# Performance work log

Hardware: AMD Instinct MI355X
Metric: run time of the kernel (lower is better)

The kernel has to match this reference:

```python
import jax, jax.numpy as jnp
import numpy as np

THRESHOLD_P = 0.4  # nucleus_select default threshold_p


def setup_inputs() -> dict:
    key = jax.random.key(0)
    B, N = 512, 50257
    logits = jax.random.normal(key, (B, N), dtype=jnp.float32)
    # nucleus_select consumes softmax weights (rows sum to 1)
    weights = jax.nn.softmax(logits, axis=-1)
    return {"weights": weights}


def reference(weights):
    """Batched nucleus (top-p) selection, jit-compatible padded form.

    Returns:
      sorted_idx: (B, N) int32  -- indices of weights sorted descending
      norm_w:     (B, N) f32    -- renormalized selected weights in sorted
                                   order; positions >= k are exactly 0
      k:          (B,)   int32  -- nucleus size per sample (>= 1)
    For sample b the torch module's outputs are sorted_idx[b, :k[b]] and
    norm_w[b, :k[b]].
    """
    B, N = weights.shape
    # descending sort (values + original indices)
    sorted_idx = jnp.argsort(-weights, axis=-1)
    sorted_w = jnp.take_along_axis(weights, sorted_idx, axis=-1)
    cumsum = jnp.cumsum(sorted_w, axis=-1)
    exceeded = cumsum > THRESHOLD_P
    # first position where cumsum > p, then +1; if never exceeded, keep all N
    first = jnp.argmax(exceeded, axis=-1).astype(jnp.int32)
    k = jnp.where(jnp.any(exceeded, axis=-1), first + 1, jnp.int32(N))
    k = jnp.maximum(k, 1)
    keep = jnp.arange(N, dtype=jnp.int32)[None, :] < k[:, None]  # (B, N)
    sel_w = sorted_w * keep.astype(sorted_w.dtype)
    norm_w = sel_w / jnp.sum(sel_w, axis=-1, keepdims=True)
    return sorted_idx.astype(jnp.int32), norm_w, k
```

## Files before the change

### kernel.cpp

```cpp
#include <hip/hip_runtime.h>
#include <stdint.h>

#define B    512
#define N    50257
#define BLK  512
#define NWAVE 8
#define TILE 5632
#define CHUNK 704
#define NGRP 11
#define THRESH 0.4f

__device__ __forceinline__ uint32_t sort_key(float w) { return ~__float_as_uint(w); }

__device__ __forceinline__ void hist_elem(uint32_t* hw0, const float w) {
    const uint32_t key = sort_key(w);
    atomicAdd(hw0 + (key & 255u), 1u);
    atomicAdd(hw0 + 256 + ((key >> 8) & 255u), 1u);
    atomicAdd(hw0 + 512 + ((key >> 16) & 255u), 1u);
    atomicAdd(hw0 + 768 + ((key >> 24) & 255u), 1u);
}

__global__ __launch_bounds__(BLK) void hist4_fast(const float* __restrict__ wts,
                                                  uint32_t* __restrict__ histWS) {
    __shared__ uint32_t hw[NWAVE][4][256];
    __shared__ uint32_t wtot[4];
    const int row = blockIdx.x;
    const size_t base = (size_t)row * N;
    const int tid = threadIdx.x;
    const int lane = tid & 63;
    const int wv = tid >> 6;

    {
        uint32_t* p = &hw[wv][0][0];
        for (int j = lane; j < 4 * 256; j += 64) p[j] = 0;
    }
    uint32_t* hw0 = &hw[wv][0][0];

    const int head = (int)((4 - (base & 3)) & 3);
    for (int i = tid; i < head; i += BLK) hist_elem(hw0, wts[base + i]);
    const int nvec = (N - head) >> 2;
    const float4* v4 = (const float4*)(wts + base + head);
    for (int iv = tid; iv < nvec; iv += BLK) {
        const float4 f = v4[iv];
        hist_elem(hw0, f.x); hist_elem(hw0, f.y);
        hist_elem(hw0, f.z); hist_elem(hw0, f.w);
    }
    for (int i = head + 4 * nvec + tid; i < N; i += BLK) hist_elem(hw0, wts[base + i]);
    __syncthreads();

    for (int p = 0; p < 4; ++p) {
        uint32_t cnt = 0;
        if (tid < 256) {
            #pragma unroll
            for (int w = 0; w < NWAVE; ++w) cnt += hw[w][p][tid];
        }
        uint32_t incl = cnt;
        #pragma unroll
        for (int o = 1; o < 64; o <<= 1) {
            const uint32_t u = __shfl_up(incl, o);
            if (lane >= o) incl += u;
        }
        if (tid < 256 && lane == 63) wtot[tid >> 6] = incl;
        __syncthreads();
        if (tid < 256) {
            uint32_t prefix = 0;
            const int w4 = tid >> 6;
            #pragma unroll
            for (int w2 = 0; w2 < 4; ++w2) if (w2 < w4) prefix += wtot[w2];
            histWS[((size_t)row * 4 + p) * 256 + tid] = prefix + incl - cnt;
        }
        __syncthreads();
    }
}

template <int SHIFT, bool FIRST, bool LAST>
__global__ __launch_bounds__(BLK, 4) void scatter_pl(const float* __restrict__ wts,
                                                     const unsigned long long* __restrict__ src,
                                                     unsigned long long* __restrict__ dst,
                                                     uint32_t* __restrict__ outIdx,
                                                     float* __restrict__ outW,
                                                     const uint32_t* __restrict__ histWS) {
    __shared__ __align__(16) unsigned long long stage[TILE];
    __shared__ uint16_t waveCnt[NWAVE][256];
    __shared__ uint32_t delta[256];
    __shared__ uint32_t wtot[4];

    const int row = blockIdx.x;
    const size_t base = (size_t)row * N;
    const int tid  = threadIdx.x;
    const int lane = tid & 63;
    const int wv   = tid >> 6;
    constexpr int PASS = SHIFT / 8;
    constexpr int KS = SHIFT + 16;

    uint32_t curReg = 0;
    if (tid < 256) curReg = histWS[((size_t)row * 4 + PASS) * 256 + tid];

    const int numTiles = (N + TILE - 1) / TILE;

    unsigned long long pairN[NGRP];
    {
        const int cb = wv * CHUNK;
        #pragma unroll
        for (int g = 0; g < NGRP; ++g) {
            const int i = cb + g * 64 + lane;
            pairN[g] = FIRST ? (((unsigned long long)sort_key(wts[base + i]) << 16) | (uint32_t)i)
                             : src[base + i];
        }
    }

    for (int t = 0; t < numTiles; ++t) {
        const int tbase = t * TILE;
        const int tileLen = (N - tbase < TILE) ? (N - tbase) : TILE;
        const int cbase = tbase + wv * CHUNK;
        const bool full = (tbase + TILE <= N);

        {
            uint2* z = (uint2*)&waveCnt[wv][0];
            z[lane] = make_uint2(0u, 0u);
        }
        unsigned long long pairR[NGRP];
        uint32_t posR[NGRP];
        #pragma unroll
        for (int g = 0; g < NGRP; ++g) pairR[g] = pairN[g];

        if (full) {
            #pragma unroll
            for (int g = 0; g < NGRP; ++g) {
                const uint32_t d = (uint32_t)(pairR[g] >> KS) & 255u;
                unsigned long long peers = ~0ull;
                #pragma unroll
                for (int bb = 0; bb < 8; ++bb) {
                    const unsigned long long bit = __ballot((d >> bb) & 1u);
                    peers &= ((d >> bb) & 1u) ? bit : ~bit;
                }
                const unsigned long long lower = peers & ((1ull << lane) - 1ull);
                const uint32_t cnt = (uint32_t)waveCnt[wv][d];
                posR[g] = cnt + (uint32_t)__popcll(lower);
                if (lower == 0ull) waveCnt[wv][d] = (uint16_t)(cnt + (uint32_t)__popcll(peers));
            }
        } else {
            #pragma unroll
            for (int g = 0; g < NGRP; ++g) {
                const int i = cbase + g * 64 + lane;
                const bool valid = (i < N);
                const uint32_t d = (uint32_t)(pairR[g] >> KS) & 255u;
                unsigned long long peers = __ballot(valid);
                #pragma unroll
                for (int bb = 0; bb < 8; ++bb) {
                    const unsigned long long bit = __ballot((d >> bb) & 1u);
                    peers &= ((d >> bb) & 1u) ? bit : ~bit;
                }
                const unsigned long long lower = peers & ((1ull << lane) - 1ull);
                uint32_t cnt = 0;
                if (valid) cnt = (uint32_t)waveCnt[wv][d];
                posR[g] = cnt + (uint32_t)__popcll(lower);
                if (valid && lower == 0ull) waveCnt[wv][d] = (uint16_t)(cnt + (uint32_t)__popcll(peers));
            }
        }
        __syncthreads();

        uint32_t run = 0;
        if (tid < 256) {
            #pragma unroll
            for (int w = 0; w < NWAVE; ++w) {
                const uint32_t c = (uint32_t)waveCnt[w][tid];
                waveCnt[w][tid] = (uint16_t)run;
                run += c;
            }
        }
        uint32_t incl = run;
        #pragma unroll
        for (int o = 1; o < 64; o <<= 1) {
            const uint32_t u = __shfl_up(incl, o);
            if (lane >= o) incl += u;
        }
        if (tid < 256 && lane == 63) wtot[tid >> 6] = incl;
        __syncthreads();
        if (tid < 256) {
            uint32_t prefix = 0;
            const int w4 = tid >> 6;
            #pragma unroll
            for (int w2 = 0; w2 < 4; ++w2) if (w2 < w4) prefix += wtot[w2];
            const uint32_t ts = prefix + incl - run;
            delta[tid] = curReg - ts;
            curReg += run;
            #pragma unroll
            for (int w = 0; w < NWAVE; ++w)
                waveCnt[w][tid] = (uint16_t)((uint32_t)waveCnt[w][tid] + ts);
        }
        __syncthreads();

        if (t + 1 < numTiles) {
            const int ncb = (t + 1) * TILE + wv * CHUNK;
            if (ncb + CHUNK <= N) {
                #pragma unroll
                for (int g = 0; g < NGRP; ++g) {
                    const int i = ncb + g * 64 + lane;
                    pairN[g] = FIRST ? (((unsigned long long)sort_key(wts[base + i]) << 16) | (uint32_t)i)
                                     : src[base + i];
                }
            } else {
                #pragma unroll
                for (int g = 0; g < NGRP; ++g) {
                    const int i = ncb + g * 64 + lane;
                    unsigned long long pair = 0;
                    if (i < N)
                        pair = FIRST ? (((unsigned long long)sort_key(wts[base + i]) << 16) | (uint32_t)i)
                                     : src[base + i];
                    pairN[g] = pair;
                }
            }
        }

        if (full) {
            #pragma unroll
            for (int g = 0; g < NGRP; ++g) {
                const uint32_t d = (uint32_t)(pairR[g] >> KS) & 255u;
                stage[(uint32_t)waveCnt[wv][d] + posR[g]] = pairR[g];
            }
        } else {
            #pragma unroll
            for (int g = 0; g < NGRP; ++g) {
                const int i = cbase + g * 64 + lane;
                if (i < N) {
                    const uint32_t d = (uint32_t)(pairR[g] >> KS) & 255u;
                    stage[(uint32_t)waveCnt[wv][d] + posR[g]] = pairR[g];
                }
            }
        }
        __syncthreads();

        const int tileLenEven = tileLen & ~1;
        for (int p0 = 2 * tid; p0 < tileLenEven; p0 += 2 * BLK) {
            const ulonglong2 two = *(const ulonglong2*)&stage[p0];
            const uint32_t d0 = (uint32_t)(two.x >> KS) & 255u;
            const uint32_t d1 = (uint32_t)(two.y >> KS) & 255u;
            const uint32_t g0 = delta[d0] + (uint32_t)p0;
            const uint32_t g1 = delta[d1] + (uint32_t)p0 + 1u;
            if (LAST) {
                outIdx[base + g0] = (uint32_t)(two.x & 0xFFFFull);
                outW[base + g0]   = __uint_as_float(~(uint32_t)(two.x >> 16));
                outIdx[base + g1] = (uint32_t)(two.y & 0xFFFFull);
                outW[base + g1]   = __uint_as_float(~(uint32_t)(two.y >> 16));
            } else {
                dst[base + g0] = two.x;
                dst[base + g1] = two.y;
            }
        }
        for (int p = tileLenEven + tid; p < tileLen; p += BLK) {
            const unsigned long long pair = stage[p];
            const uint32_t d = (uint32_t)(pair >> KS) & 255u;
            const uint32_t g = delta[d] + (uint32_t)p;
            if (LAST) {
                outIdx[base + g] = (uint32_t)(pair & 0xFFFFull);
                outW[base + g]   = __uint_as_float(~(uint32_t)(pair >> 16));
            } else {
                dst[base + g] = pair;
            }
        }
    }
}

__global__ __launch_bounds__(BLK) void finalize_row(float* __restrict__ out0,
                                                    float* __restrict__ out1,
                                                    float* __restrict__ out2) {
    __shared__ float waveSum[NWAVE];
    __shared__ int   waveFirst[NWAVE];
    __shared__ float waveCum[NWAVE];
    __shared__ int   s_k;
    __shared__ float s_total;

    const int row = blockIdx.x;
    const size_t base = (size_t)row * N;
    const int tid  = threadIdx.x;
    const int lane = tid & 63;
    const int wv   = tid >> 6;

    if (tid == 0) { s_k = -1; s_total = 0.f; }
    __syncthreads();

    float carry = 0.f;
    const int numTiles = (N + BLK - 1) / BLK;
    for (int t = 0; t < numTiles; ++t) {
        const int i = t * BLK + tid;
        const bool valid = (i < N);
        float w = valid ? out1[base + i] : 0.f;

        float s = w;
        #pragma unroll
        for (int o = 1; o < 64; o <<= 1) {
            float u = __shfl_up(s, o);
            if (lane >= o) s += u;
        }
        if (lane == 63) waveSum[wv] = s;
        __syncthreads();

        float prefix = 0.f, blockTot = 0.f;
        #pragma unroll
        for (int w2 = 0; w2 < NWAVE; ++w2) {
            float t2 = waveSum[w2];
            if (w2 < wv) prefix += t2;
            blockTot += t2;
        }
        const float cum = carry + prefix + s;

        const bool exceed = valid && (cum > THRESH);
        const unsigned long long bal = __ballot(exceed);
        const int fl = (bal == 0ull) ? 64 : (__ffsll(bal) - 1);
        if (lane == 0) waveFirst[wv] = fl;
        if (fl < 64 && lane == fl) waveCum[wv] = cum;
        __syncthreads();
        if (tid == 0) {
            for (int w2 = 0; w2 < NWAVE; ++w2) {
                if (waveFirst[w2] < 64) {
                    s_k = t * BLK + w2 * 64 + waveFirst[w2] + 1;
                    s_total = waveCum[w2];
                    break;
                }
            }
        }
        __syncthreads();
        if (s_k >= 0) break;
        carry += blockTot;
        __syncthreads();
    }

    int k = s_k;
    float total = s_total;
    if (k < 0) { k = N; total = carry; }
    const float inv = 1.0f / total;

    const uint32_t* idxU = (const uint32_t*)out0;
    const int head = (int)((4 - (base & 3)) & 3);
    const int nvec = (N - head) >> 2;
    const int vend = head + 4 * nvec;

    for (int i = tid; i < head; i += BLK) {
        const uint32_t idx = idxU[base + i];
        const float w = out1[base + i];
        out0[base + i] = (float)idx;
        out1[base + i] = (i < k) ? (w * inv) : 0.f;
    }
    const uint4*  ivp = (const uint4*)(idxU + base + head);
    float4*       o0v = (float4*)(out0 + base + head);
    float4*       o1v = (float4*)(out1 + base + head);
    for (int v = tid; v < nvec; v += BLK) {
        const uint4  iv = ivp[v];
        const float4 wv4 = o1v[v];
        const int i = head + 4 * v;
        float4 o0, o1;
        o0.x = (float)iv.x; o0.y = (float)iv.y; o0.z = (float)iv.z; o0.w = (float)iv.w;
        o1.x = (i + 0 < k) ? wv4.x * inv : 0.f;
        o1.y = (i + 1 < k) ? wv4.y * inv : 0.f;
        o1.z = (i + 2 < k) ? wv4.z * inv : 0.f;
        o1.w = (i + 3 < k) ? wv4.w * inv : 0.f;
        o0v[v] = o0;
        o1v[v] = o1;
    }
    for (int i = vend + tid; i < N; i += BLK) {
        const uint32_t idx = idxU[base + i];
        const float w = out1[base + i];
        out0[base + i] = (float)idx;
        out1[base + i] = (i < k) ? (w * inv) : 0.f;
    }
    if (tid == 0) out2[row] = (float)k;
}

#define NSUB (TILE / BLK)

template <int SHIFT, bool FIRST, bool LAST>
__global__ __launch_bounds__(BLK, 4) void scatter_tile(const float* __restrict__ wts,
                                                       const uint32_t* __restrict__ keySrc,
                                                       const uint16_t* __restrict__ idxSrc,
                                                       uint32_t* __restrict__ keyDst,
                                                       uint16_t* __restrict__ idxDst,
                                                       uint32_t* __restrict__ outIdx,
                                                       float* __restrict__ outW,
                                                       const uint32_t* __restrict__ histWS) {
    __shared__ uint32_t stageKey[TILE];
    __shared__ uint16_t stageIdx[TILE];
    __shared__ uint32_t waveCnt32[NWAVE][256];
    __shared__ uint16_t subOff[NSUB][256];
    __shared__ uint32_t cursor[256];
    __shared__ uint32_t tileCnt[256];
    __shared__ uint32_t tileStart[256];
    __shared__ uint32_t scanb[256];

    const int row = blockIdx.x;
    const size_t base = (size_t)row * N;
    const int tid  = threadIdx.x;
    const int lane = tid & 63;
    const int wv   = tid >> 6;
    constexpr int PASS = SHIFT / 8;

    if (tid < 256) cursor[tid] = histWS[((size_t)row * 4 + PASS) * 256 + tid];

    const int numTiles = (N + TILE - 1) / TILE;
    for (int t = 0; t < numTiles; ++t) {
        const int tbase = t * TILE;
        const int tileLen = (N - tbase < TILE) ? (N - tbase) : TILE;

        uint32_t keyR[NSUB];
        uint32_t idxR[NSUB];
        uint32_t posR[NSUB];

        #pragma unroll
        for (int s = 0; s < NSUB; ++s) {
            for (int j = tid; j < NWAVE * 256; j += BLK) ((uint32_t*)waveCnt32)[j] = 0;
            __syncthreads();

            const int i = tbase + s * BLK + tid;
            const bool valid = (i < N);
            uint32_t key = 0, idx = 0, d = 0;
            if (valid) {
                if (FIRST) { key = sort_key(wts[base + i]); idx = (uint32_t)i; }
                else       { key = keySrc[base + i]; idx = (uint32_t)idxSrc[base + i]; }
                d = (key >> SHIFT) & 255u;
            }
            keyR[s] = key;
            if (!FIRST) idxR[s] = idx;

            unsigned long long peers = __ballot(valid);
            #pragma unroll
            for (int b = 0; b < 8; ++b) {
                unsigned long long bit = __ballot(valid && ((d >> b) & 1u));
                peers &= ((d >> b) & 1u) ? bit : ~bit;
            }
            const unsigned long long lower = peers & ((1ull << lane) - 1ull);
            const uint32_t rank = (uint32_t)__popcll(lower);
            if (valid && lower == 0ull) waveCnt32[wv][d] = (uint32_t)__popcll(peers);
            __syncthreads();

            if (tid < 256) {
                uint32_t x = 0;
                #pragma unroll
                for (int w = 0; w < NWAVE; ++w) {
                    uint32_t c = waveCnt32[w][tid];
                    waveCnt32[w][tid] = x;
                    x += c;
                }
                subOff[s][tid] = (uint16_t)x;
            }
            __syncthreads();

            posR[s] = valid ? (waveCnt32[wv][d] + rank) : 0u;
            __syncthreads();
        }

        if (tid < 256) {
            uint32_t run = 0;
            #pragma unroll
            for (int s = 0; s < NSUB; ++s) {
                uint32_t c = subOff[s][tid];
                subOff[s][tid] = (uint16_t)run;
                run += c;
            }
            tileCnt[tid] = run;
            scanb[tid] = run;
        }
        __syncthreads();
        for (int off = 1; off < 256; off <<= 1) {
            uint32_t add = 0;
            if (tid < 256 && tid >= off) add = scanb[tid - off];
            __syncthreads();
            if (tid < 256) scanb[tid] += add;
            __syncthreads();
        }
        if (tid < 256) tileStart[tid] = (tid == 0) ? 0u : scanb[tid - 1];
        __syncthreads();

        #pragma unroll
        for (int s = 0; s < NSUB; ++s) {
            const int i = tbase + s * BLK + tid;
            if (i < N) {
                const uint32_t d = (keyR[s] >> SHIFT) & 255u;
                const uint32_t pos = tileStart[d] + (uint32_t)subOff[s][d] + posR[s];
                stageKey[pos] = keyR[s];
                stageIdx[pos] = (uint16_t)(FIRST ? (uint32_t)i : idxR[s]);
            }
        }
        __syncthreads();

        for (int p = tid; p < tileLen; p += BLK) {
            const uint32_t k = stageKey[p];
            const uint32_t d = (k >> SHIFT) & 255u;
            const uint32_t g = cursor[d] + (uint32_t)p - tileStart[d];
            if (LAST) {
                outIdx[base + g] = (uint32_t)stageIdx[p];
                outW[base + g]   = __uint_as_float(~k);
            } else {
                keyDst[base + g] = k;
                idxDst[base + g] = stageIdx[p];
            }
        }
        __syncthreads();
        if (tid < 256) cursor[tid] += tileCnt[tid];
        __syncthreads();
    }
}

template <int SHIFT>
__global__ __launch_bounds__(BLK) void radix_pass_fb(const float* __restrict__ wts,
                                                     const uint32_t* __restrict__ src,
                                                     uint32_t* __restrict__ dst) {
    __shared__ uint32_t hist[256];
    __shared__ uint32_t scanb[256];
    __shared__ uint32_t running[256];
    __shared__ uint32_t waveCnt32[NWAVE][256];

    const int row = blockIdx.x;
    const size_t base = (size_t)row * N;
    const int tid  = threadIdx.x;
    const int lane = tid & 63;
    const int wv   = tid >> 6;

    if (tid < 256) hist[tid] = 0;
    __syncthreads();
    for (int i = tid; i < N; i += BLK) {
        uint32_t idx = (SHIFT == 0) ? (uint32_t)i : src[base + i];
        uint32_t d = (sort_key(wts[base + idx]) >> SHIFT) & 255u;
        atomicAdd(&hist[d], 1u);
    }
    __syncthreads();

    if (tid < 256) scanb[tid] = hist[tid];
    __syncthreads();
    for (int off = 1; off < 256; off <<= 1) {
        uint32_t add = 0;
        if (tid < 256 && tid >= off) add = scanb[tid - off];
        __syncthreads();
        if (tid < 256) scanb[tid] += add;
        __syncthreads();
    }
    if (tid < 256) running[tid] = (tid == 0) ? 0u : scanb[tid - 1];
    __syncthreads();

    const int numTiles = (N + BLK - 1) / BLK;
    for (int t = 0; t < numTiles; ++t) {
        for (int j = tid; j < NWAVE * 256; j += BLK) ((uint32_t*)waveCnt32)[j] = 0;
        __syncthreads();

        const int i = t * BLK + tid;
        const bool valid = (i < N);
        uint32_t idx = 0, d = 0;
        if (valid) {
            idx = (SHIFT == 0) ? (uint32_t)i : src[base + i];
            d = (sort_key(wts[base + idx]) >> SHIFT) & 255u;
        }
        unsigned long long peers = __ballot(valid);
        #pragma unroll
        for (int b = 0; b < 8; ++b) {
            unsigned long long bit = __ballot(valid && ((d >> b) & 1u));
            peers &= ((d >> b) & 1u) ? bit : ~bit;
        }
        const unsigned long long lower = peers & ((1ull << lane) - 1ull);
        const uint32_t rank = (uint32_t)__popcll(lower);
        if (valid && lower == 0ull) waveCnt32[wv][d] = (uint32_t)__popcll(peers);
        __syncthreads();

        if (tid < 256) {
            uint32_t s = running[tid];
            #pragma unroll
            for (int w = 0; w < NWAVE; ++w) {
                uint32_t c = waveCnt32[w][tid];
                waveCnt32[w][tid] = s;
                s += c;
            }
            running[tid] = s;
        }
        __syncthreads();

        if (valid) {
            uint32_t pos = waveCnt32[wv][d] + rank;
            dst[base + pos] = idx;
        }
        __syncthreads();
    }
}

__global__ __launch_bounds__(BLK) void finalize_fb(const float* __restrict__ wts,
                                                   const uint32_t* __restrict__ sidx,
                                                   float* __restrict__ out0,
                                                   float* __restrict__ out1,
                                                   float* __restrict__ out2) {
    __shared__ float waveSum[NWAVE];
    __shared__ int   waveFirst[NWAVE];
    __shared__ float waveCum[NWAVE];
    __shared__ int   s_k;
    __shared__ float s_total;

    const int row = blockIdx.x;
    const size_t base = (size_t)row * N;
    const int tid  = threadIdx.x;
    const int lane = tid & 63;
    const int wv   = tid >> 6;

    if (tid == 0) { s_k = -1; s_total = 0.f; }
    __syncthreads();

    float carry = 0.f;
    const int numTiles = (N + BLK - 1) / BLK;
    for (int t = 0; t < numTiles; ++t) {
        const int i = t * BLK + tid;
        const bool valid = (i < N);
        float w = valid ? wts[base + sidx[base + i]] : 0.f;

        float s = w;
        #pragma unroll
        for (int o = 1; o < 64; o <<= 1) {
            float u = __shfl_up(s, o);
            if (lane >= o) s += u;
        }
        if (lane == 63) waveSum[wv] = s;
        __syncthreads();

        float prefix = 0.f, blockTot = 0.f;
        #pragma unroll
        for (int w2 = 0; w2 < NWAVE; ++w2) {
            float t2 = waveSum[w2];
            if (w2 < wv) prefix += t2;
            blockTot += t2;
        }
        const float cum = carry + prefix + s;

        const bool exceed = valid && (cum > THRESH);
        const unsigned long long bal = __ballot(exceed);
        const int fl = (bal == 0ull) ? 64 : (__ffsll(bal) - 1);
        if (lane == 0) waveFirst[wv] = fl;
        if (fl < 64 && lane == fl) waveCum[wv] = cum;
        __syncthreads();
        if (tid == 0) {
            for (int w2 = 0; w2 < NWAVE; ++w2) {
                if (waveFirst[w2] < 64) {
                    s_k = t * BLK + w2 * 64 + waveFirst[w2] + 1;
                    s_total = waveCum[w2];
                    break;
                }
            }
        }
        __syncthreads();
        if (s_k >= 0) break;
        carry += blockTot;
        __syncthreads();
    }

    int k = s_k;
    float total = s_total;
    if (k < 0) { k = N; total = carry; }

    for (int i = tid; i < N; i += BLK) {
        const uint32_t idx = sidx[base + i];
        const float w = wts[base + idx];
        out0[base + i] = (float)idx;
        out1[base + i] = (i < k) ? (w / total) : 0.f;
    }
    if (tid == 0) out2[row] = (float)k;
}


extern "C" void kernel_launch(void* const* d_in, const int* in_sizes, int n_in,
                              void* d_out, int out_size, void* d_ws, size_t ws_size,
                              hipStream_t stream) {
    const float* wts = (const float*)d_in[0];
    float* out0 = (float*)d_out;
    float* out1 = out0 + (size_t)B * N;
    float* out2 = out0 + 2 * (size_t)B * N;

    const size_t PAIR_BYTES = (size_t)B * N * 8;
    const size_t KEY_BYTES  = (size_t)B * N * 4;
    const size_t IDX_BYTES  = (size_t)B * N * 2;
    const size_t HIST_BYTES = (size_t)B * 4 * 256 * 4;
    const size_t WS_A = PAIR_BYTES + HIST_BYTES;
    const size_t WS_B = KEY_BYTES + IDX_BYTES + HIST_BYTES;

    dim3 g(B), b(BLK);
    if (ws_size >= WS_A) {
        uint8_t* ws = (uint8_t*)d_ws;
        unsigned long long* pairWS  = (unsigned long long*)ws;
        uint32_t*           histWS  = (uint32_t*)(ws + PAIR_BYTES);
        unsigned long long* pairOUT = (unsigned long long*)d_out;

        hist4_fast<<<g, b, 0, stream>>>(wts, histWS);
        scatter_pl<0,  true,  false><<<g, b, 0, stream>>>(wts, nullptr, pairWS, nullptr, nullptr, histWS);
        scatter_pl<8,  false, false><<<g, b, 0, stream>>>(nullptr, pairWS, pairOUT, nullptr, nullptr, histWS);
        scatter_pl<16, false, false><<<g, b, 0, stream>>>(nullptr, pairOUT, pairWS, nullptr, nullptr, histWS);
        scatter_pl<24, false, true ><<<g, b, 0, stream>>>(nullptr, pairWS, nullptr, (uint32_t*)out0, out1, histWS);
        finalize_row<<<g, b, 0, stream>>>(out0, out1, out2);
    } else if (ws_size >= WS_B) {
        uint8_t* ws = (uint8_t*)d_ws;
        uint32_t* keyWS  = (uint32_t*)ws;
        uint16_t* idxWS  = (uint16_t*)(ws + KEY_BYTES);
        uint32_t* histWS = (uint32_t*)(ws + KEY_BYTES + IDX_BYTES);
        uint32_t* keyOUT = (uint32_t*)out0;
        uint16_t* idxOUT = (uint16_t*)out1;

        hist4_fast<<<g, b, 0, stream>>>(wts, histWS);
        scatter_tile<0,  true,  false><<<g, b, 0, stream>>>(wts, nullptr, nullptr, keyWS, idxWS, nullptr, nullptr, histWS);
        scatter_tile<8,  false, false><<<g, b, 0, stream>>>(wts, keyWS, idxWS, keyOUT, idxOUT, nullptr, nullptr, histWS);
        scatter_tile<16, false, false><<<g, b, 0, stream>>>(wts, keyOUT, idxOUT, keyWS, idxWS, nullptr, nullptr, histWS);
        scatter_tile<24, false, true ><<<g, b, 0, stream>>>(wts, keyWS, idxWS, nullptr, nullptr, (uint32_t*)out0, out1, histWS);
        finalize_row<<<g, b, 0, stream>>>(out0, out1, out2);
    } else {
        uint32_t* bufA = (uint32_t*)out0;
        uint32_t* bufB = (uint32_t*)out1;
        radix_pass_fb<0 ><<<g, b, 0, stream>>>(wts, nullptr, bufA);
        radix_pass_fb<8 ><<<g, b, 0, stream>>>(wts, bufA, bufB);
        radix_pass_fb<16><<<g, b, 0, stream>>>(wts, bufB, bufA);
        radix_pass_fb<24><<<g, b, 0, stream>>>(wts, bufA, bufB);
        finalize_fb<<<g, b, 0, stream>>>(wts, bufB, out0, out1, out2);
    }
}
```

Measured before the change: 626.8 us.

## Split each row's radix scatter passes across two blocks using per-segment digit counts

Each LSD radix scatter pass now runs two blocks per row. Each block handles one segment of tiles, and the second segment's starting offsets are shifted by the first segment's digit counts. Those counts are computed in the histogram kernel for the first pass and gathered with shared and global atomics during each scatter for the next pass. The goal is to double the parallelism, since only 512 long serial blocks ran before; tiles are also smaller to allow higher occupancy. The cost is extra atomics, an added memset, and a larger workspace requirement.

Measured after the change: 742.0 us. 18.4% more time.

```diff
diff --git a/kernel.cpp b/kernel.cpp
--- a/kernel.cpp
+++ b/kernel.cpp
@@ -5,24 +5,31 @@
 #define N    50257
 #define BLK  512
 #define NWAVE 8
-#define TILE 5632
-#define CHUNK 704
-#define NGRP 11
+#define TILE 4096
+#define CHUNK 512
+#define NGRP 8
+#define NT_TOTAL 13
+#define SEG0_T 7
+#define SEGBOUND (SEG0_T * TILE)
 #define THRESH 0.4f
 
 __device__ __forceinline__ uint32_t sort_key(float w) { return ~__float_as_uint(w); }
 
-__device__ __forceinline__ void hist_elem(uint32_t* hw0, const float w) {
+__device__ __forceinline__ void hist_elem2(uint32_t* hw0, uint32_t* hs,
+                                           const float w, const bool inSeg0) {
     const uint32_t key = sort_key(w);
     atomicAdd(hw0 + (key & 255u), 1u);
     atomicAdd(hw0 + 256 + ((key >> 8) & 255u), 1u);
     atomicAdd(hw0 + 512 + ((key >> 16) & 255u), 1u);
     atomicAdd(hw0 + 768 + ((key >> 24) & 255u), 1u);
+    if (inSeg0) atomicAdd(hs + (key & 255u), 1u);
 }
 
 __global__ __launch_bounds__(BLK) void hist4_fast(const float* __restrict__ wts,
-                                                  uint32_t* __restrict__ histWS) {
+                                                  uint32_t* __restrict__ histWS,
+                                                  uint32_t* __restrict__ segCnt0) {
     __shared__ uint32_t hw[NWAVE][4][256];
+    __shared__ uint32_t hseg[NWAVE][256];
     __shared__ uint32_t wtot[4];
     const int row = blockIdx.x;
     const size_t base = (size_t)row * N;
@@ -33,20 +40,34 @@
     {
         uint32_t* p = &hw[wv][0][0];
         for (int j = lane; j < 4 * 256; j += 64) p[j] = 0;
+        uint32_t* q = &hseg[wv][0];
+        for (int j = lane; j < 256; j += 64) q[j] = 0;
     }
     uint32_t* hw0 = &hw[wv][0][0];
+    uint32_t* hs  = &hseg[wv][0];
 
     const int head = (int)((4 - (base & 3)) & 3);
-    for (int i = tid; i < head; i += BLK) hist_elem(hw0, wts[base + i]);
+    for (int i = tid; i < head; i += BLK) hist_elem2(hw0, hs, wts[base + i], i < SEGBOUND);
     const int nvec = (N - head) >> 2;
     const float4* v4 = (const float4*)(wts + base + head);
     for (int iv = tid; iv < nvec; iv += BLK) {
         const float4 f = v4[iv];
-        hist_elem(hw0, f.x); hist_elem(hw0, f.y);
-        hist_elem(hw0, f.z); hist_elem(hw0, f.w);
-    }
-    for (int i = head + 4 * nvec + tid; i < N; i += BLK) hist_elem(hw0, wts[base + i]);
+        const int p0 = head + 4 * iv;
+        hist_elem2(hw0, hs, f.x, p0 + 0 < SEGBOUND);
+        hist_elem2(hw0, hs, f.y, p0 + 1 < SEGBOUND);
+        hist_elem2(hw0, hs, f.z, p0 + 2 < SEGBOUND);
+        hist_elem2(hw0, hs, f.w, p0 + 3 < SEGBOUND);
+    }
+    for (int i = head + 4 * nvec + tid; i < N; i += BLK)
+        hist_elem2(hw0, hs, wts[base + i], i < SEGBOUND);
     __syncthreads();
+
+    if (tid < 256) {
+        uint32_t c = 0;
+        #pragma unroll
+        for (int w = 0; w < NWAVE; ++w) c += hseg[w][tid];
+        segCnt0[(size_t)row * 256 + tid] = c;
+    }
 
     for (int p = 0; p < 4; ++p) {
         uint32_t cnt = 0;
@@ -74,18 +95,22 @@
 }
 
 template <int SHIFT, bool FIRST, bool LAST>
-__global__ __launch_bounds__(BLK, 4) void scatter_pl(const float* __restrict__ wts,
-                                                     const unsigned long long* __restrict__ src,
-                                                     unsigned long long* __restrict__ dst,
-                                                     uint32_t* __restrict__ outIdx,
-                                                     float* __restrict__ outW,
-                                                     const uint32_t* __restrict__ histWS) {
+__global__ __launch_bounds__(BLK, 8) void scatter_seg(const float* __restrict__ wts,
+                                                      const unsigned long long* __restrict__ src,
+                                                      unsigned long long* __restrict__ dst,
+                                                      uint32_t* __restrict__ outIdx,
+                                                      float* __restrict__ outW,
+                                                      const uint32_t* __restrict__ histWS,
+                                                      const uint32_t* __restrict__ segCur,
+                                                      uint32_t* __restrict__ segNext) {
     __shared__ __align__(16) unsigned long long stage[TILE];
     __shared__ uint16_t waveCnt[NWAVE][256];
     __shared__ uint32_t delta[256];
+    __shared__ uint32_t cnt0[256];
     __shared__ uint32_t wtot[4];
 
     const int row = blockIdx.x;
+    const int seg = blockIdx.y;
     const size_t base = (size_t)row * N;
     const int tid  = threadIdx.x;
     const int lane = tid & 63;
@@ -93,14 +118,19 @@
     constexpr int PASS = SHIFT / 8;
     constexpr int KS = SHIFT + 16;
 
+    const int t0 = seg ? SEG0_T : 0;
+    const int t1 = seg ? NT_TOTAL : SEG0_T;
+
     uint32_t curReg = 0;
-    if (tid < 256) curReg = histWS[((size_t)row * 4 + PASS) * 256 + tid];
-
-    const int numTiles = (N + TILE - 1) / TILE;
+    if (tid < 256) {
+        curReg = histWS[((size_t)row * 4 + PASS) * 256 + tid];
+        if (seg) curReg += segCur[(size_t)row * 256 + tid];
+        cnt0[tid] = 0;
+    }
 
     unsigned long long pairN[NGRP];
     {
-        const int cb = wv * CHUNK;
+        const int cb = t0 * TILE + wv * CHUNK;
         #pragma unroll
         for (int g = 0; g < NGRP; ++g) {
             const int i = cb + g * 64 + lane;
@@ -109,7 +139,7 @@
         }
     }
 
-    for (int t = 0; t < numTiles; ++t) {
+    for (int t = t0; t < t1; ++t) {
         const int tbase = t * TILE;
         const int tileLen = (N - tbase < TILE) ? (N - tbase) : TILE;
         const int cbase = tbase + wv * CHUNK;
@@ -191,7 +221,7 @@
         }
         __syncthreads();
 
-        if (t + 1 < numTiles) {
+        if (t + 1 < t1) {
             const int ncb = (t + 1) * TILE + wv * CHUNK;
             if (ncb + CHUNK <= N) {
                 #pragma unroll
@@ -246,6 +276,8 @@
             } else {
                 dst[base + g0] = two.x;
                 dst[base + g1] = two.y;
+                if (g0 < SEGBOUND) atomicAdd(&cnt0[(uint32_t)(two.x >> (KS + 8)) & 255u], 1u);
+                if (g1 < SEGBOUND) atomicAdd(&cnt0[(uint32_t)(two.y >> (KS + 8)) & 255u], 1u);
             }
         }
         for (int p = tileLenEven + tid; p < tileLen; p += BLK) {
@@ -257,7 +289,16 @@
                 outW[base + g]   = __uint_as_float(~(uint32_t)(pair >> 16));
             } else {
                 dst[base + g] = pair;
-            }
+                if (g < SEGBOUND) atomicAdd(&cnt0[(uint32_t)(pair >> (KS + 8)) & 255u], 1u);
+            }
+        }
+    }
+
+    if (!LAST) {
+        __syncthreads();
+        if (tid < 256) {
+            const uint32_t c = cnt0[tid];
+            if (c) atomicAdd(&segNext[(size_t)row * 256 + tid], c);
         }
     }
 }
@@ -671,31 +712,41 @@
     const size_t KEY_BYTES  = (size_t)B * N * 4;
     const size_t IDX_BYTES  = (size_t)B * N * 2;
     const size_t HIST_BYTES = (size_t)B * 4 * 256 * 4;
-    const size_t WS_A = PAIR_BYTES + HIST_BYTES;
-    const size_t WS_B = KEY_BYTES + IDX_BYTES + HIST_BYTES;
+    const size_t SEG_BYTES  = (size_t)4 * B * 256 * 4;
+    const size_t WS_A = PAIR_BYTES + HIST_BYTES + SEG_BYTES;
+    const size_t WS_B = KEY_BYTES + IDX_BYTES + HIST_BYTES + SEG_BYTES;
 
     dim3 g(B), b(BLK);
     if (ws_size >= WS_A) {
         uint8_t* ws = (uint8_t*)d_ws;
         unsigned long long* pairWS  = (unsigned long long*)ws;
         uint32_t*           histWS  = (uint32_t*)(ws + PAIR_BYTES);
+        uint32_t*           segCnt  = (uint32_t*)(ws + PAIR_BYTES + HIST_BYTES);
         unsigned long long* pairOUT = (unsigned long long*)d_out;
-
-        hist4_fast<<<g, b, 0, stream>>>(wts, histWS);
-        scatter_pl<0,  true,  false><<<g, b, 0, stream>>>(wts, nullptr, pairWS, nullptr, nullptr, histWS);
-        scatter_pl<8,  false, false><<<g, b, 0, stream>>>(nullptr, pairWS, pairOUT, nullptr, nullptr, histWS);
-        scatter_pl<16, false, false><<<g, b, 0, stream>>>(nullptr, pairOUT, pairWS, nullptr, nullptr, histWS);
-        scatter_pl<24, false, true ><<<g, b, 0, stream>>>(nullptr, pairWS, nullptr, (uint32_t*)out0, out1, histWS);
+        uint32_t* seg0 = segCnt;
+        uint32_t* seg1 = segCnt + (size_t)B * 256;
+        uint32_t* seg2 = segCnt + 2 * (size_t)B * 256;
+        uint32_t* seg3 = segCnt + 3 * (size_t)B * 256;
+
+        hipMemsetAsync(seg1, 0, 3 * (size_t)B * 256 * 4, stream);
+
+        dim3 g2(B, 2);
+        hist4_fast<<<g, b, 0, stream>>>(wts, histWS, seg0);
+        scatter_seg<0,  true,  false><<<g2, b, 0, stream>>>(wts, nullptr, pairWS, nullptr, nullptr, histWS, seg0, seg1);
+        scatter_seg<8,  false, false><<<g2, b, 0, stream>>>(nullptr, pairWS, pairOUT, nullptr, nullptr, histWS, seg1, seg2);
+        scatter_seg<16, false, false><<<g2, b, 0, stream>>>(nullptr, pairOUT, pairWS, nullptr, nullptr, histWS, seg2, seg3);
+        scatter_seg<24, false, true ><<<g2, b, 0, stream>>>(nullptr, pairWS, nullptr, (uint32_t*)out0, out1, histWS, seg3, nullptr);
         finalize_row<<<g, b, 0, stream>>>(out0, out1, out2);
     } else if (ws_size >= WS_B) {
         uint8_t* ws = (uint8_t*)d_ws;
         uint32_t* keyWS  = (uint32_t*)ws;
         uint16_t* idxWS  = (uint16_t*)(ws + KEY_BYTES);
         uint32_t* histWS = (uint32_t*)(ws + KEY_BYTES + IDX_BYTES);
+        uint32_t* segWS  = (uint32_t*)(ws + KEY_BYTES + IDX_BYTES + HIST_BYTES);
         uint32_t* keyOUT = (uint32_t*)out0;
         uint16_t* idxOUT = (uint16_t*)out1;
 
-        hist4_fast<<<g, b, 0, stream>>>(wts, histWS);
+        hist4_fast<<<g, b, 0, stream>>>(wts, histWS, segWS);
         scatter_tile<0,  true,  false><<<g, b, 0, stream>>>(wts, nullptr, nullptr, keyWS, idxWS, nullptr, nullptr, histWS);
         scatter_tile<8,  false, false><<<g, b, 0, stream>>>(wts, keyWS, idxWS, keyOUT, idxOUT, nullptr, nullptr, histWS);
         scatter_tile<16, false, false><<<g, b, 0, stream>>>(wts, keyOUT, idxOUT, keyWS, idxWS, nullptr, nullptr, histWS);
```
